# Kernel optimization log

Hardware: AMD Instinct MI355X
Metric: run time of the kernel (lower is better)

The kernel has to match this reference:

```python
import jax, jax.numpy as jnp
from jax import lax
import numpy as np

DN = ('NHWC', 'HWIO', 'NHWC')
BN_EPS = 1e-3  # keras BatchNormalization default epsilon
# 91 threshold candidates, identical to np.arange(0, 0.91, 0.01) in otsu()
THRESH = jnp.asarray(np.arange(0.0, 0.91, 0.01), dtype=jnp.float32)


def _conv(x, w, b, s):
    return lax.conv_general_dilated(x, w, (s, s), 'SAME', dimension_numbers=DN) + b


def _convT(x, w, b, s):
    return lax.conv_transpose(x, w, (s, s), 'SAME', dimension_numbers=DN) + b


def _bn(x, p):
    g, be, m, v = p  # gamma, beta, moving_mean, moving_var (inference mode)
    return (x - m) * lax.rsqrt(v + BN_EPS) * g + be


def _otsu(error):
    # Vectorized equivalent of the nested-python-loop otsu(): for each batch
    # element, find eps in THRESH maximizing p0*p1*(mean0-mean1)^2 where
    # class0 = {err < eps}. Implemented as histogram + cumsums + argmax.
    B, n, m = error.shape
    N = n * m
    K = THRESH.shape[0]
    nb = K + 1  # bin K holds err >= THRESH[-1]
    e = error.reshape(B, N)
    # bins[b,i] = #{k : THRESH[k] <= e[b,i]}  =>  (e < THRESH[k]) <=> (bins <= k)
    bins = jnp.searchsorted(THRESH, e, side='right')
    seg = (jnp.arange(B)[:, None] * nb + bins).reshape(-1)
    counts = jax.ops.segment_sum(jnp.ones(B * N, jnp.float32), seg,
                                 num_segments=B * nb).reshape(B, nb)
    sums = jax.ops.segment_sum(e.reshape(-1), seg,
                               num_segments=B * nb).reshape(B, nb)
    c0 = jnp.cumsum(counts, axis=1)[:, :K]   # |class0| per threshold
    s0 = jnp.cumsum(sums, axis=1)[:, :K]     # sum(class0) per threshold
    tot = jnp.sum(sums, axis=1, keepdims=True)
    p0 = c0 / N
    p1 = 1.0 - p0
    mean0 = s0 / jnp.maximum(c0, 1.0)
    mean1 = (tot - s0) / jnp.maximum(N - c0, 1.0)
    sigma_w = jnp.where((c0 > 0) & (c0 < N), p0 * p1 * (mean0 - mean1) ** 2, 0.0)
    # strict-improvement loop == first argmax; all-zero sigma => threshold 0.0
    return THRESH[jnp.argmax(sigma_w, axis=1)]


def reference(x, eps_z,
              e_w1, e_b1, e_bn1, e_w2, e_b2, e_bn2, e_w3, e_b3, e_bn3,
              e_wm, e_bm, e_wv, e_bv,
              d_wd, d_bd, d_w1, d_b1, d_bn1, d_w2, d_b2, d_bn2,
              d_w3, d_b3, d_bn3, d_w4, d_b4):
    # ---- encoder (Dropout is identity at inference) ----
    h = _bn(jax.nn.relu(_conv(x, e_w1, e_b1, 2)), e_bn1)   # [B,16,16,32]
    h = _bn(jax.nn.relu(_conv(h, e_w2, e_b2, 2)), e_bn2)   # [B,8,8,64]
    h = _bn(jax.nn.relu(_conv(h, e_w3, e_b3, 2)), e_bn3)   # [B,4,4,128]
    h = h.reshape(h.shape[0], -1)                           # [B,2048]
    z_mean = jax.nn.relu(h @ e_wm + e_bm)
    z_log_var = jax.nn.relu(h @ e_wv + e_bv)
    z = z_mean + jnp.exp(0.5 * z_log_var) * eps_z           # Sampling layer
    # ---- decoder ----
    d = jax.nn.relu(z @ d_wd + d_bd).reshape(-1, 8, 8, 128)
    d = _bn(jax.nn.relu(_convT(d, d_w1, d_b1, 1)), d_bn1)   # [B,8,8,128]
    d = _bn(jax.nn.relu(_convT(d, d_w2, d_b2, 2)), d_bn2)   # [B,16,16,64]
    d = _bn(jax.nn.relu(_convT(d, d_w3, d_b3, 2)), d_bn3)   # [B,32,32,32]
    recon = jax.nn.sigmoid(_convT(d, d_w4, d_b4, 1))        # [B,32,32,3]
    # ---- per-pixel error + Otsu threshold + discriminative labelling ----
    error = jnp.mean((x - recon) ** 2, axis=-1)             # [B,32,32]
    thr = _otsu(error)                                      # [B]
    mask = (error < thr[:, None, None]).astype(jnp.int32)   # [B,32,32]
    return mask


def setup_inputs() -> dict:
    key = jax.random.key(0)
    ks = jax.random.split(key, 12)
    B = 2048
    p = lambda k, s: 0.05 * jax.random.normal(k, s, jnp.float32)
    bn = lambda c: (jnp.ones(c, jnp.float32), jnp.zeros(c, jnp.float32),
                    jnp.zeros(c, jnp.float32), jnp.ones(c, jnp.float32))
    return dict(
        x=jax.random.uniform(ks[0], (B, 32, 32, 3), jnp.float32),
        eps_z=jax.random.normal(ks[1], (B, 128), jnp.float32),
        e_w1=p(ks[2], (5, 5, 3, 32)), e_b1=jnp.zeros(32, jnp.float32), e_bn1=bn(32),
        e_w2=p(ks[3], (5, 5, 32, 64)), e_b2=jnp.zeros(64, jnp.float32), e_bn2=bn(64),
        e_w3=p(ks[4], (5, 5, 64, 128)), e_b3=jnp.zeros(128, jnp.float32), e_bn3=bn(128),
        e_wm=p(ks[5], (2048, 128)), e_bm=jnp.zeros(128, jnp.float32),
        e_wv=p(ks[6], (2048, 128)), e_bv=jnp.zeros(128, jnp.float32),
        d_wd=p(ks[7], (128, 8192)), d_bd=jnp.zeros(8192, jnp.float32),
        d_w1=p(ks[8], (1, 1, 128, 128)), d_b1=jnp.zeros(128, jnp.float32), d_bn1=bn(128),
        d_w2=p(ks[9], (3, 3, 128, 64)), d_b2=jnp.zeros(64, jnp.float32), d_bn2=bn(64),
        d_w3=p(ks[10], (3, 3, 64, 32)), d_b3=jnp.zeros(32, jnp.float32), d_bn3=bn(32),
        d_w4=p(ks[11], (3, 3, 32, 3)), d_b4=jnp.zeros(3, jnp.float32),
    )
```

## Files before the change

### kernel.cpp

```cpp
#include <hip/hip_runtime.h>
#include <math.h>

#define B_TOTAL 2048


__device__ __forceinline__ float bn_fold_scale(float g, float v) {
    return g * (float)(1.0 / sqrt((double)v + 1e-3));
}

__global__ __launch_bounds__(256) void k_conv1(
    const float* __restrict__ x, const float* __restrict__ w,
    const float* __restrict__ bias,
    const float* __restrict__ g, const float* __restrict__ be,
    const float* __restrict__ mm, const float* __restrict__ vv,
    float* __restrict__ out, int b0)
{
    __shared__ __align__(16) float sIn[3072];
    __shared__ __align__(16) float sW[2400];
    __shared__ __align__(16) float sB[32], sS[32], sBi[32];
    int t = threadIdx.x;
    const float* xin = x + (size_t)(b0 + blockIdx.x) * 3072;
    for (int i = t; i < 3072; i += 256) sIn[i] = xin[i];
    for (int i = t; i < 2400; i += 256) sW[i] = w[i];
    if (t < 32) {
        float sc = bn_fold_scale(g[t], vv[t]);
        sS[t] = sc; sBi[t] = be[t] - mm[t] * sc; sB[t] = bias[t];
    }
    __syncthreads();
    int oy = t >> 4, ox = t & 15;
    float patch[75];
#pragma unroll
    for (int kh = 0; kh < 5; ++kh) {
        int iy = 2 * oy - 1 + kh;
#pragma unroll
        for (int kw = 0; kw < 5; ++kw) {
            int ix = 2 * ox - 1 + kw;
            bool v = ((unsigned)iy < 32u) && ((unsigned)ix < 32u);
            int base = (iy * 32 + ix) * 3;
#pragma unroll
            for (int c = 0; c < 3; ++c)
                patch[(kh * 5 + kw) * 3 + c] = v ? sIn[base + c] : 0.0f;
        }
    }
    float acc[32];
#pragma unroll
    for (int i = 0; i < 32; ++i) acc[i] = 0.0f;
#pragma unroll 5
    for (int i = 0; i < 75; ++i) {
        float v = patch[i];
        const float* wr = &sW[i * 32];
#pragma unroll
        for (int q = 0; q < 8; ++q) {
            float wl[4];
            *(float4*)wl = *(const float4*)&wr[q * 4];
            acc[q*4+0] = fmaf(v, wl[0], acc[q*4+0]);
            acc[q*4+1] = fmaf(v, wl[1], acc[q*4+1]);
            acc[q*4+2] = fmaf(v, wl[2], acc[q*4+2]);
            acc[q*4+3] = fmaf(v, wl[3], acc[q*4+3]);
        }
    }
    float* o = out + ((size_t)blockIdx.x * 256 + t) * 32;
#pragma unroll
    for (int q = 0; q < 8; ++q) {
        float ov[4];
#pragma unroll
        for (int j = 0; j < 4; ++j) {
            int c = q * 4 + j;
            float r = fmaxf(acc[c] + sB[c], 0.0f);
            ov[j] = fmaf(r, sS[c], sBi[c]);
        }
        *(float4*)&o[q * 4] = *(float4*)ov;
    }
}

__global__ __launch_bounds__(256) void k_c2g(
    const float* __restrict__ in, const float* __restrict__ w,
    const float* __restrict__ bias,
    const float* __restrict__ g, const float* __restrict__ be,
    const float* __restrict__ mm, const float* __restrict__ vv,
    float* __restrict__ out)
{
    __shared__ __align__(16) float sA[32 * 132];
    __shared__ __align__(16) float sW[32 * 64];
    __shared__ __align__(16) float sB[64], sS[64], sBi[64];
    int t = threadIdx.x;
    int img0 = blockIdx.x * 2;
    if (t < 64) {
        float sc = bn_fold_scale(g[t], vv[t]);
        sS[t] = sc; sBi[t] = be[t] - mm[t] * sc; sB[t] = bias[t];
    }
    const float* in0 = in + (size_t)img0 * 8192;
    int tx = t & 15, ty = t >> 4;
    float acc[8][4];
#pragma unroll
    for (int i = 0; i < 8; ++i)
#pragma unroll
        for (int j = 0; j < 4; ++j) acc[i][j] = 0.0f;

    for (int tap = 0; tap < 25; ++tap) {
        int kh = tap / 5, kw = tap - kh * 5;
        __syncthreads();
        for (int i = t; i < 4096; i += 256) {
            int ci = i & 31, m = i >> 5;
            int im = m >> 6, pix = m & 63;
            int oy = pix >> 3, ox = pix & 7;
            int iy = 2 * oy - 1 + kh, ix = 2 * ox - 1 + kw;
            float v = ((unsigned)iy < 16u && (unsigned)ix < 16u)
                          ? in0[((size_t)im * 256 + iy * 16 + ix) * 32 + ci] : 0.0f;
            sA[ci * 132 + m] = v;
        }
        for (int i = t; i < 2048; i += 256) {
            int co = i & 63, ci = i >> 6;
            sW[ci * 64 + co] = w[((size_t)tap * 32 + ci) * 64 + co];
        }
        __syncthreads();
#pragma unroll 4
        for (int ci = 0; ci < 32; ++ci) {
            float b[4];
            *(float4*)b = *(const float4*)&sW[ci * 64 + tx * 4];
            float a0[4], a1[4];
            *(float4*)a0 = *(const float4*)&sA[ci * 132 + ty * 8];
            *(float4*)a1 = *(const float4*)&sA[ci * 132 + ty * 8 + 4];
#pragma unroll
            for (int mi = 0; mi < 4; ++mi)
#pragma unroll
                for (int j = 0; j < 4; ++j) {
                    acc[mi][j]     = fmaf(a0[mi], b[j], acc[mi][j]);
                    acc[4 + mi][j] = fmaf(a1[mi], b[j], acc[4 + mi][j]);
                }
        }
    }
    int c0 = tx * 4;
    float sc[4], bi[4], bv[4];
#pragma unroll
    for (int j = 0; j < 4; ++j) { sc[j] = sS[c0 + j]; bi[j] = sBi[c0 + j]; bv[j] = sB[c0 + j]; }
#pragma unroll
    for (int mi = 0; mi < 8; ++mi) {
        int m = ty * 8 + mi;
        int im = m >> 6, pix = m & 63;
        float ov[4];
#pragma unroll
        for (int j = 0; j < 4; ++j) {
            float r = fmaxf(acc[mi][j] + bv[j], 0.0f);
            ov[j] = fmaf(r, sc[j], bi[j]);
        }
        *(float4*)&out[((size_t)(img0 + im) * 64 + pix) * 64 + c0] = *(float4*)ov;
    }
}

__global__ __launch_bounds__(256) void k_c3g(
    const float* __restrict__ in, const float* __restrict__ w,
    const float* __restrict__ bias,
    const float* __restrict__ g, const float* __restrict__ be,
    const float* __restrict__ mm, const float* __restrict__ vv,
    float* __restrict__ out)
{
    __shared__ __align__(16) float sA[64 * 68];
    __shared__ __align__(16) float sW[64 * 128];
    __shared__ __align__(16) float sB[128], sS[128], sBi[128];
    int t = threadIdx.x;
    int img0 = blockIdx.x * 4;
    if (t < 128) {
        float sc = bn_fold_scale(g[t], vv[t]);
        sS[t] = sc; sBi[t] = be[t] - mm[t] * sc; sB[t] = bias[t];
    }
    const float* in0 = in + (size_t)img0 * 4096;
    int tx = t & 15, ty = t >> 4;
    float acc[4][8];
#pragma unroll
    for (int i = 0; i < 4; ++i)
#pragma unroll
        for (int j = 0; j < 8; ++j) acc[i][j] = 0.0f;

    for (int tap = 0; tap < 25; ++tap) {
        int kh = tap / 5, kw = tap - kh * 5;
        __syncthreads();
        for (int i = t; i < 4096; i += 256) {
            int ci = i & 63, m = i >> 6;
            int im = m >> 4, pix = m & 15;
            int oy = pix >> 2, ox = pix & 3;
            int iy = 2 * oy - 1 + kh, ix = 2 * ox - 1 + kw;
            float v = ((unsigned)iy < 8u && (unsigned)ix < 8u)
                          ? in0[((size_t)im * 64 + iy * 8 + ix) * 64 + ci] : 0.0f;
            sA[ci * 68 + m] = v;
        }
        for (int i = t; i < 8192; i += 256) {
            int co = i & 127, ci = i >> 7;
            sW[ci * 128 + co] = w[((size_t)tap * 64 + ci) * 128 + co];
        }
        __syncthreads();
#pragma unroll 2
        for (int ci = 0; ci < 64; ++ci) {
            float b[8];
            *(float4*)&b[0] = *(const float4*)&sW[ci * 128 + tx * 4];
            *(float4*)&b[4] = *(const float4*)&sW[ci * 128 + 64 + tx * 4];
            float a[4];
            *(float4*)a = *(const float4*)&sA[ci * 68 + ty * 4];
#pragma unroll
            for (int mi = 0; mi < 4; ++mi)
#pragma unroll
                for (int j = 0; j < 8; ++j)
                    acc[mi][j] = fmaf(a[mi], b[j], acc[mi][j]);
        }
    }
    int cA = tx * 4, cB = 64 + tx * 4;
#pragma unroll
    for (int mi = 0; mi < 4; ++mi) {
        int m = ty * 4 + mi;
        int im = m >> 4, pix = m & 15;
        float* o = &out[((size_t)(img0 + im) * 16 + pix) * 128];
        float ov0[4], ov1[4];
#pragma unroll
        for (int j = 0; j < 4; ++j) {
            float r = fmaxf(acc[mi][j] + sB[cA + j], 0.0f);
            ov0[j] = fmaf(r, sS[cA + j], sBi[cA + j]);
        }
#pragma unroll
        for (int j = 0; j < 4; ++j) {
            float r = fmaxf(acc[mi][4 + j] + sB[cB + j], 0.0f);
            ov1[j] = fmaf(r, sS[cB + j], sBi[cB + j]);
        }
        *(float4*)&o[cA] = *(float4*)ov0;
        *(float4*)&o[cB] = *(float4*)ov1;
    }
}

__global__ __launch_bounds__(256) void k_zpart(
    const float* __restrict__ A, const float* __restrict__ Wm,
    const float* __restrict__ Wv, float* __restrict__ part)
{
    __shared__ __align__(16) float sA[16 * 33];
    __shared__ __align__(16) float sW[32 * 256];
    int t = threadIdx.x;
    int img0 = blockIdx.x * 16;
    int k00 = blockIdx.y * 256;
    int li = t >> 4, cg = t & 15;
    float acc[16];
#pragma unroll
    for (int i = 0; i < 16; ++i) acc[i] = 0.0f;
    for (int k0 = 0; k0 < 256; k0 += 32) {
        for (int i = t; i < 512; i += 256) {
            int r = i >> 5, k = i & 31;
            sA[r * 33 + k] = A[(size_t)(img0 + r) * 2048 + k00 + k0 + k];
        }
        for (int i = t; i < 8192; i += 256) {
            int k = i >> 8, c = i & 255;
            float v = (c < 128) ? Wm[(size_t)(k00 + k0 + k) * 128 + c]
                                : Wv[(size_t)(k00 + k0 + k) * 128 + (c - 128)];
            sW[k * 256 + c] = v;
        }
        __syncthreads();
#pragma unroll 4
        for (int k = 0; k < 32; ++k) {
            float a = sA[li * 33 + k];
            const float* wr = &sW[k * 256];
#pragma unroll
            for (int q = 0; q < 4; ++q) {
                float wl[4];
                *(float4*)wl = *(const float4*)&wr[q * 64 + cg * 4];
                acc[q*4+0] = fmaf(a, wl[0], acc[q*4+0]);
                acc[q*4+1] = fmaf(a, wl[1], acc[q*4+1]);
                acc[q*4+2] = fmaf(a, wl[2], acc[q*4+2]);
                acc[q*4+3] = fmaf(a, wl[3], acc[q*4+3]);
            }
        }
        __syncthreads();
    }
    float* p = part + ((size_t)(img0 + li) * 8 + blockIdx.y) * 256;
#pragma unroll
    for (int q = 0; q < 4; ++q) {
        float4 v = make_float4(acc[q*4], acc[q*4+1], acc[q*4+2], acc[q*4+3]);
        *(float4*)&p[q * 64 + cg * 4] = v;
    }
}

__global__ __launch_bounds__(256) void k_zcombine(
    const float* __restrict__ part, const float* __restrict__ bm,
    const float* __restrict__ bv, const float* __restrict__ eps,
    float* __restrict__ z, int b0)
{
    int idx = blockIdx.x * 256 + threadIdx.x;
    int img = idx >> 7, c = idx & 127;
    const float* p = part + (size_t)img * 2048;
    float sm = 0.f, sv = 0.f;
#pragma unroll
    for (int s = 0; s < 8; ++s) { sm += p[s * 256 + c]; sv += p[s * 256 + 128 + c]; }
    float zm = fmaxf(sm + bm[c], 0.0f);
    float zlv = fmaxf(sv + bv[c], 0.0f);
    z[idx] = zm + expf(0.5f * zlv) * eps[(size_t)(b0 + img) * 128 + c];
}

__global__ __launch_bounds__(256) void k_gemm128(
    const float* __restrict__ A, const float* __restrict__ W,
    const float* __restrict__ bias,
    const float* __restrict__ g, const float* __restrict__ be,
    const float* __restrict__ mm, const float* __restrict__ vv,
    float* __restrict__ out, int N, int M)
{
    __shared__ __align__(16) float sAt[64 * 68];
    __shared__ __align__(16) float sB[64 * 68];
    int t = threadIdx.x;
    int tx = t & 15, ty = t >> 4;
    int row0 = blockIdx.x * 64, col0 = blockIdx.y * 64;
    float acc[16];
#pragma unroll
    for (int i = 0; i < 16; ++i) acc[i] = 0.0f;
    for (int kc = 0; kc < 128; kc += 64) {
        for (int i = t; i < 4096; i += 256) {
            int r = i >> 6, k = i & 63;
            sAt[k * 68 + r] = (row0 + r < M) ? A[(size_t)(row0 + r) * 128 + kc + k] : 0.0f;
        }
        for (int i = t; i < 4096; i += 256) {
            int k = i >> 6, c = i & 63;
            sB[k * 68 + c] = W[(size_t)(kc + k) * N + col0 + c];
        }
        __syncthreads();
#pragma unroll 8
        for (int k = 0; k < 64; ++k) {
            float a[4], b[4];
            *(float4*)a = *(const float4*)&sAt[k * 68 + ty * 4];
            *(float4*)b = *(const float4*)&sB[k * 68 + tx * 4];
#pragma unroll
            for (int i = 0; i < 4; ++i)
#pragma unroll
                for (int j = 0; j < 4; ++j)
                    acc[i * 4 + j] = fmaf(a[i], b[j], acc[i * 4 + j]);
        }
        __syncthreads();
    }
    int c0 = col0 + tx * 4;
    float bvv[4];
    *(float4*)bvv = *(const float4*)&bias[c0];
    float sc[4], bi[4];
    bool has_bn = (g != nullptr);
    if (has_bn) {
#pragma unroll
        for (int j = 0; j < 4; ++j) {
            float s = bn_fold_scale(g[c0 + j], vv[c0 + j]);
            sc[j] = s; bi[j] = be[c0 + j] - mm[c0 + j] * s;
        }
    }
#pragma unroll
    for (int i = 0; i < 4; ++i) {
        int row = row0 + ty * 4 + i;
        if (row >= M) continue;
        float ov[4];
#pragma unroll
        for (int j = 0; j < 4; ++j) {
            float r = fmaxf(acc[i * 4 + j] + bvv[j], 0.0f);
            ov[j] = has_bn ? fmaf(r, sc[j], bi[j]) : r;
        }
        *(float4*)&out[(size_t)row * N + c0] = *(float4*)ov;
    }
}

template <int RY, int RX>
__device__ __forceinline__ void ct2g_body(
    const float* __restrict__ in0, const float* __restrict__ w,
    float* __restrict__ sA, float* __restrict__ sW,
    const float* __restrict__ sB, const float* __restrict__ sS,
    const float* __restrict__ sBi, float* __restrict__ out0)
{
    constexpr int NTY = RY ? 1 : 2;
    constexpr int NTX = RX ? 1 : 2;
    constexpr int TT = NTY * NTX;
    int t = threadIdx.x;
    int px0 = (t & 1) * 4;
    int py  = (t >> 1) & 7;
    int u   = (t >> 4) & 1;
    int ty  = t >> 5;
    int co0 = ty * 8;
    int imgA = 2 * u, imgB = 2 * u + 1;
    float acc0[4][8], acc1[4][8];
#pragma unroll
    for (int i = 0; i < 4; ++i)
#pragma unroll
        for (int j = 0; j < 8; ++j) { acc0[i][j] = 0.0f; acc1[i][j] = 0.0f; }

    for (int pass = 0; pass < 8; ++pass) {
        int ci0 = pass * 16;
        __syncthreads();
        for (int img = 0; img < 4; ++img) {
            const float* xin = in0 + (size_t)img * 8192;
            for (int i = t; i < 16 * 81; i += 256) {
                int ci = i & 15, pix = i >> 4;
                int r = pix / 9, c = pix - r * 9;
                int iy = r - 1, ix = c - 1;
                float v = (iy >= 0 && ix >= 0) ? xin[(iy * 8 + ix) * 128 + ci0 + ci] : 0.0f;
                sA[(img * 16 + ci) * 81 + pix] = v;
            }
        }
        for (int tb = 0; tb < TT; tb += 2) {
            if (tb) __syncthreads();
            for (int i = t; i < 2 * 16 * 64; i += 256) {
                int kk = i >> 6, co = i & 63;
                int tl = kk >> 4, ci = kk & 15;
                int tt = tb + tl; if (tt >= TT) tt = TT - 1;
                int kh = RY ? 1 : 2 * (tt / NTX);
                int kw = RX ? 1 : 2 * (tt % NTX);
                sW[kk * 64 + co] = w[((size_t)(kh * 3 + kw) * 128 + ci0 + ci) * 64 + co];
            }
            __syncthreads();
#pragma unroll
            for (int tl = 0; tl < 2; ++tl) {
                int tt = tb + tl;
                if (tt >= TT) break;
                int tY = tt / NTX, tX = tt % NTX;
                int r = RY ? (py + 1) : (py + tY);
                int cb = RX ? (px0 + 1) : (px0 + tX);
                int aB = r * 9 + cb;
#pragma unroll 4
                for (int ci = 0; ci < 16; ++ci) {
                    float b[8];
                    *(float4*)&b[0] = *(const float4*)&sW[(tl * 16 + ci) * 64 + co0];
                    *(float4*)&b[4] = *(const float4*)&sW[(tl * 16 + ci) * 64 + co0 + 4];
                    float a0[4], a1[4];
                    const float* pA = &sA[(imgA * 16 + ci) * 81 + aB];
                    const float* pB = &sA[(imgB * 16 + ci) * 81 + aB];
                    a0[0] = pA[0]; a0[1] = pA[1]; a0[2] = pA[2]; a0[3] = pA[3];
                    a1[0] = pB[0]; a1[1] = pB[1]; a1[2] = pB[2]; a1[3] = pB[3];
#pragma unroll
                    for (int i = 0; i < 4; ++i)
#pragma unroll
                        for (int j = 0; j < 8; ++j) {
                            acc0[i][j] = fmaf(a0[i], b[j], acc0[i][j]);
                            acc1[i][j] = fmaf(a1[i], b[j], acc1[i][j]);
                        }
                }
            }
        }
    }
#pragma unroll
    for (int l = 0; l < 2; ++l) {
        int img = 2 * u + l;
        float* oimg = out0 + (size_t)img * 16384;
#pragma unroll
        for (int i = 0; i < 4; ++i) {
            int oy = 2 * py + RY, ox = 2 * (px0 + i) + RX;
            float* o = oimg + (oy * 16 + ox) * 64 + co0;
            float ov0[4], ov1[4];
#pragma unroll
            for (int j = 0; j < 4; ++j) {
                int c = co0 + j;
                float r = fmaxf((l ? acc1[i][j] : acc0[i][j]) + sB[c], 0.0f);
                ov0[j] = fmaf(r, sS[c], sBi[c]);
            }
#pragma unroll
            for (int j = 0; j < 4; ++j) {
                int c = co0 + 4 + j;
                float r = fmaxf((l ? acc1[i][4 + j] : acc0[i][4 + j]) + sB[c], 0.0f);
                ov1[j] = fmaf(r, sS[c], sBi[c]);
            }
            *(float4*)o = *(float4*)ov0;
            *(float4*)(o + 4) = *(float4*)ov1;
        }
    }
}

__global__ __launch_bounds__(256, 4) void k_ct2g(
    const float* __restrict__ in, const float* __restrict__ w,
    const float* __restrict__ bias,
    const float* __restrict__ g, const float* __restrict__ be,
    const float* __restrict__ mm, const float* __restrict__ vv,
    float* __restrict__ out)
{
    __shared__ __align__(16) float sA[4 * 16 * 81];
    __shared__ __align__(16) float sW[2 * 16 * 64];
    __shared__ __align__(16) float sB[64], sS[64], sBi[64];
    int t = threadIdx.x;
    if (t < 64) {
        float sc = bn_fold_scale(g[t], vv[t]);
        sS[t] = sc; sBi[t] = be[t] - mm[t] * sc; sB[t] = bias[t];
    }
    const float* in0 = in + (size_t)blockIdx.x * 4 * 8192;
    float* out0 = out + (size_t)blockIdx.x * 4 * 16384;
    switch (blockIdx.y) {
        case 0:  ct2g_body<0,0>(in0, w, sA, sW, sB, sS, sBi, out0); break;
        case 1:  ct2g_body<0,1>(in0, w, sA, sW, sB, sS, sBi, out0); break;
        case 2:  ct2g_body<1,0>(in0, w, sA, sW, sB, sS, sBi, out0); break;
        default: ct2g_body<1,1>(in0, w, sA, sW, sB, sS, sBi, out0); break;
    }
}

template <int RY, int RX>
__device__ __forceinline__ void ct3g_body(
    const float* __restrict__ in0, const float* __restrict__ w,
    float* __restrict__ sA, float* __restrict__ sW,
    const float* __restrict__ sB, const float* __restrict__ sS,
    const float* __restrict__ sBi, float* __restrict__ out0)
{
    constexpr int NTY = RY ? 1 : 2;
    constexpr int NTX = RX ? 1 : 2;
    constexpr int TT = NTY * NTX;
    int t = threadIdx.x;
    int px0 = (t & 3) * 4;
    int py  = (t >> 2) & 15;
    int ty  = t >> 6;
    int co0 = ty * 8;
    float acc0[4][8], acc1[4][8];
#pragma unroll
    for (int i = 0; i < 4; ++i)
#pragma unroll
        for (int j = 0; j < 8; ++j) { acc0[i][j] = 0.0f; acc1[i][j] = 0.0f; }

    for (int pass = 0; pass < 8; ++pass) {
        int ci0 = pass * 8;
        __syncthreads();
        for (int img = 0; img < 2; ++img) {
            const float* xin = in0 + (size_t)img * 16384;
            for (int i = t; i < 8 * 289; i += 256) {
                int ci = i & 7, pix = i >> 3;
                int r = pix / 17, c = pix - r * 17;
                int iy = r - 1, ix = c - 1;
                float v = (iy >= 0 && ix >= 0) ? xin[(iy * 16 + ix) * 64 + ci0 + ci] : 0.0f;
                sA[(img * 8 + ci) * 289 + pix] = v;
            }
        }
        for (int tb = 0; tb < TT; tb += 2) {
            if (tb) __syncthreads();
            for (int i = t; i < 2 * 8 * 32; i += 256) {
                int kk = i >> 5, co = i & 31;
                int tl = kk >> 3, ci = kk & 7;
                int tt = tb + tl; if (tt >= TT) tt = TT - 1;
                int kh = RY ? 1 : 2 * (tt / NTX);
                int kw = RX ? 1 : 2 * (tt % NTX);
                sW[kk * 32 + co] = w[((size_t)(kh * 3 + kw) * 64 + ci0 + ci) * 32 + co];
            }
            __syncthreads();
#pragma unroll
            for (int tl = 0; tl < 2; ++tl) {
                int tt = tb + tl;
                if (tt >= TT) break;
                int tY = tt / NTX, tX = tt % NTX;
                int r = RY ? (py + 1) : (py + tY);
                int cb = RX ? (px0 + 1) : (px0 + tX);
                int aB = r * 17 + cb;
#pragma unroll 4
                for (int ci = 0; ci < 8; ++ci) {
                    float b[8];
                    *(float4*)&b[0] = *(const float4*)&sW[(tl * 8 + ci) * 32 + co0];
                    *(float4*)&b[4] = *(const float4*)&sW[(tl * 8 + ci) * 32 + co0 + 4];
                    float a0[4], a1[4];
                    const float* pA = &sA[ci * 289 + aB];
                    const float* pB = &sA[(8 + ci) * 289 + aB];
                    a0[0] = pA[0]; a0[1] = pA[1]; a0[2] = pA[2]; a0[3] = pA[3];
                    a1[0] = pB[0]; a1[1] = pB[1]; a1[2] = pB[2]; a1[3] = pB[3];
#pragma unroll
                    for (int i = 0; i < 4; ++i)
#pragma unroll
                        for (int j = 0; j < 8; ++j) {
                            acc0[i][j] = fmaf(a0[i], b[j], acc0[i][j]);
                            acc1[i][j] = fmaf(a1[i], b[j], acc1[i][j]);
                        }
                }
            }
        }
    }
#pragma unroll
    for (int l = 0; l < 2; ++l) {
        float* oimg = out0 + (size_t)l * 32768;
#pragma unroll
        for (int i = 0; i < 4; ++i) {
            int oy = 2 * py + RY, ox = 2 * (px0 + i) + RX;
            float* o = oimg + (oy * 32 + ox) * 32 + co0;
            float ov0[4], ov1[4];
#pragma unroll
            for (int j = 0; j < 4; ++j) {
                int c = co0 + j;
                float r = fmaxf((l ? acc1[i][j] : acc0[i][j]) + sB[c], 0.0f);
                ov0[j] = fmaf(r, sS[c], sBi[c]);
            }
#pragma unroll
            for (int j = 0; j < 4; ++j) {
                int c = co0 + 4 + j;
                float r = fmaxf((l ? acc1[i][4 + j] : acc0[i][4 + j]) + sB[c], 0.0f);
                ov1[j] = fmaf(r, sS[c], sBi[c]);
            }
            *(float4*)o = *(float4*)ov0;
            *(float4*)(o + 4) = *(float4*)ov1;
        }
    }
}

__global__ __launch_bounds__(256, 4) void k_ct3g(
    const float* __restrict__ in, const float* __restrict__ w,
    const float* __restrict__ bias,
    const float* __restrict__ g, const float* __restrict__ be,
    const float* __restrict__ mm, const float* __restrict__ vv,
    float* __restrict__ out)
{
    __shared__ __align__(16) float sA[2 * 8 * 289];
    __shared__ __align__(16) float sW[2 * 8 * 32];
    __shared__ __align__(16) float sB[32], sS[32], sBi[32];
    int t = threadIdx.x;
    if (t < 32) {
        float sc = bn_fold_scale(g[t], vv[t]);
        sS[t] = sc; sBi[t] = be[t] - mm[t] * sc; sB[t] = bias[t];
    }
    const float* in0 = in + (size_t)blockIdx.x * 2 * 16384;
    float* out0 = out + (size_t)blockIdx.x * 2 * 32768;
    switch (blockIdx.y) {
        case 0:  ct3g_body<0,0>(in0, w, sA, sW, sB, sS, sBi, out0); break;
        case 1:  ct3g_body<0,1>(in0, w, sA, sW, sB, sS, sBi, out0); break;
        case 2:  ct3g_body<1,0>(in0, w, sA, sW, sB, sS, sBi, out0); break;
        default: ct3g_body<1,1>(in0, w, sA, sW, sB, sS, sBi, out0); break;
    }
}

__global__ __launch_bounds__(256) void k_convT4_err(
    const float* __restrict__ in, const float* __restrict__ w,
    const float* __restrict__ b, const float* __restrict__ x,
    float* __restrict__ err, int b0)
{
    __shared__ __align__(16) float sIn[32 * 342];
    int t = threadIdx.x;
    int quart = blockIdx.x, img = blockIdx.y;
    int r0 = quart * 8;
    const float* xin = in + (size_t)img * 32768;
    for (int i = t; i < 10880; i += 256) {
        int pix = i >> 5, ci = i & 31;
        int lr = pix / 34;
        int cx = pix - lr * 34 - 1;
        int gy = r0 - 1 + lr;
        float v = (((unsigned)gy < 32u) && ((unsigned)cx < 32u))
                      ? xin[(gy * 32 + cx) * 32 + ci] : 0.0f;
        sIn[ci * 342 + pix] = v;
    }
    __syncthreads();
    int ly = t >> 5, lx = t & 31;
    float a0 = 0.f, a1 = 0.f, a2 = 0.f;
#pragma unroll
    for (int kh = 0; kh < 3; ++kh)
#pragma unroll
        for (int kw = 0; kw < 3; ++kw) {
            int pix = (ly + kh) * 34 + (lx + kw);
            const float* wp = w + ((kh * 3 + kw) * 32) * 3;
#pragma unroll 4
            for (int ci = 0; ci < 32; ++ci) {
                float v = sIn[ci * 342 + pix];
                a0 = fmaf(v, wp[ci * 3 + 0], a0);
                a1 = fmaf(v, wp[ci * 3 + 1], a1);
                a2 = fmaf(v, wp[ci * 3 + 2], a2);
            }
        }
    float s0 = 1.0f / (1.0f + expf(-(a0 + b[0])));
    float s1 = 1.0f / (1.0f + expf(-(a1 + b[1])));
    float s2 = 1.0f / (1.0f + expf(-(a2 + b[2])));
    int oy = r0 + ly;
    size_t xi = (((size_t)(b0 + img) * 32 + oy) * 32 + lx) * 3;
    float d0 = x[xi + 0] - s0;
    float d1 = x[xi + 1] - s1;
    float d2 = x[xi + 2] - s2;
    err[(size_t)img * 1024 + oy * 32 + lx] = (d0 * d0 + d1 * d1 + d2 * d2) * (1.0f / 3.0f);
}

__global__ __launch_bounds__(256) void k_otsu(
    const float* __restrict__ err, int* __restrict__ mask)
{
    __shared__ float sE[1024];
    __shared__ float sRed[4];
    __shared__ float sSig[96];
    __shared__ float sThr;
    int img = blockIdx.x, t = threadIdx.x;
    const float* e = err + (size_t)img * 1024;
    float part = 0.f;
    for (int i = t; i < 1024; i += 256) { float v = e[i]; sE[i] = v; part += v; }
    for (int o = 32; o; o >>= 1) part += __shfl_down(part, o);
    if ((t & 63) == 0) sRed[t >> 6] = part;
    __syncthreads();
    float tot = sRed[0] + sRed[1] + sRed[2] + sRed[3];
    if (t < 91) {
        float T = (float)((double)t * 0.01);
        int c = 0; float s = 0.f;
        for (int i = 0; i < 1024; ++i) {
            float v = sE[i];
            bool lt = v < T;
            c += lt ? 1 : 0;
            s += lt ? v : 0.0f;
        }
        float cf = (float)c;
        float p0 = cf * (1.0f / 1024.0f);
        float p1 = 1.0f - p0;
        float m0 = s / fmaxf(cf, 1.0f);
        float m1 = (tot - s) / fmaxf(1024.0f - cf, 1.0f);
        float d = m0 - m1;
        sSig[t] = (c > 0 && c < 1024) ? (p0 * p1) * (d * d) : 0.0f;
    }
    __syncthreads();
    if (t == 0) {
        float best = sSig[0]; int bk = 0;
        for (int k = 1; k < 91; ++k)
            if (sSig[k] > best) { best = sSig[k]; bk = k; }
        sThr = (float)((double)bk * 0.01);
    }
    __syncthreads();
    float thr = sThr;
    int* m = mask + (size_t)img * 1024;
    for (int i = t; i < 1024; i += 256) m[i] = (sE[i] < thr) ? 1 : 0;
}

extern "C" void kernel_launch(void* const* d_in, const int* in_sizes, int n_in,
                              void* d_out, int out_size, void* d_ws, size_t ws_size,
                              hipStream_t stream)
{
    (void)in_sizes; (void)out_size;
    const float* p[46];
    bool flat = (n_in >= 46);
    if (flat) {
        for (int i = 0; i < 46; ++i) p[i] = (const float*)d_in[i];
    } else {
        int o = 0;
        int s = 0;
        auto leaf = [&](int count) {
            for (int j = 0; j < count; ++j) p[o++] = (const float*)d_in[s++];
        };
        auto bn4 = [&](int C) {
            const float* base = (const float*)d_in[s++];
            p[o++] = base; p[o++] = base + C; p[o++] = base + 2 * C; p[o++] = base + 3 * C;
        };
        leaf(2);
        leaf(2); bn4(32);
        leaf(2); bn4(64);
        leaf(2); bn4(128);
        leaf(4);
        leaf(2);
        leaf(2); bn4(128);
        leaf(2); bn4(64);
        leaf(2); bn4(32);
        leaf(2);
    }
    const float* x      = p[0];
    const float* epsz   = p[1];
    const float* e_w1   = p[2];
    const float* e_b1   = p[3];
    const float* e_bn1g = p[4], *e_bn1b = p[5], *e_bn1m = p[6], *e_bn1v = p[7];
    const float* e_w2   = p[8];
    const float* e_b2   = p[9];
    const float* e_bn2g = p[10], *e_bn2b = p[11], *e_bn2m = p[12], *e_bn2v = p[13];
    const float* e_w3   = p[14];
    const float* e_b3   = p[15];
    const float* e_bn3g = p[16], *e_bn3b = p[17], *e_bn3m = p[18], *e_bn3v = p[19];
    const float* e_wm   = p[20];
    const float* e_bm   = p[21];
    const float* e_wv   = p[22];
    const float* e_bv   = p[23];
    const float* d_wd   = p[24];
    const float* d_bd   = p[25];
    const float* d_w1   = p[26];
    const float* d_b1   = p[27];
    const float* d_bn1g = p[28], *d_bn1b = p[29], *d_bn1m = p[30], *d_bn1v = p[31];
    const float* d_w2   = p[32];
    const float* d_b2   = p[33];
    const float* d_bn2g = p[34], *d_bn2b = p[35], *d_bn2m = p[36], *d_bn2v = p[37];
    const float* d_w3   = p[38];
    const float* d_b3   = p[39];
    const float* d_bn3g = p[40], *d_bn3b = p[41], *d_bn3m = p[42], *d_bn3v = p[43];
    const float* d_w4   = p[44];
    const float* d_b4   = p[45];
    int* mask = (int*)d_out;

    float* ws = (float*)d_ws;
    int Bc = B_TOTAL;
    while (Bc > 16) {
        size_t need = (size_t)Bc * 50304u * 4u;
        if (need <= ws_size) break;
        Bc >>= 1;
    }
    float* err = ws;
    float* z   = err + (size_t)Bc * 1024;
    float* P   = z + (size_t)Bc * 128;
    float* Q   = P + (size_t)Bc * 16384;

    for (int b0 = 0; b0 < B_TOTAL; b0 += Bc) {
        k_conv1<<<Bc, 256, 0, stream>>>(x, e_w1, e_b1, e_bn1g, e_bn1b, e_bn1m, e_bn1v, P, b0);
        k_c2g<<<Bc / 2, 256, 0, stream>>>(P, e_w2, e_b2, e_bn2g, e_bn2b, e_bn2m, e_bn2v, Q);
        k_c3g<<<Bc / 4, 256, 0, stream>>>(Q, e_w3, e_b3, e_bn3g, e_bn3b, e_bn3m, e_bn3v, P);
        k_zpart<<<dim3(Bc / 16, 8), 256, 0, stream>>>(P, e_wm, e_wv, Q);
        k_zcombine<<<(Bc * 128) / 256, 256, 0, stream>>>(Q, e_bm, e_bv, epsz, z, b0);
        k_gemm128<<<dim3((Bc + 63) / 64, 128), 256, 0, stream>>>(z, d_wd, d_bd,
            nullptr, nullptr, nullptr, nullptr, P, 8192, Bc);
        k_gemm128<<<dim3(Bc, 2), 256, 0, stream>>>(P, d_w1, d_b1,
            d_bn1g, d_bn1b, d_bn1m, d_bn1v, Q, 128, Bc * 64);
        k_ct2g<<<dim3(Bc / 4, 4), 256, 0, stream>>>(Q, d_w2, d_b2, d_bn2g, d_bn2b, d_bn2m, d_bn2v, P);
        k_ct3g<<<dim3(Bc / 2, 4), 256, 0, stream>>>(P, d_w3, d_b3, d_bn3g, d_bn3b, d_bn3m, d_bn3v, Q);
        k_convT4_err<<<dim3(4, Bc), 256, 0, stream>>>(Q, d_w4, d_b4, x, err, b0);
        k_otsu<<<Bc, 256, 0, stream>>>(err, mask + (size_t)b0 * 1024);
    }
}
```

Before: 2.246 ms.

## Prefetch next tap's conv3 input and weights into registers during compute

The conv3 kernel now loads the next tap's im2col input slice and weight slice from global memory into registers (48 floats per thread) while the current tap is being computed. The registers are stored to shared memory at the start of the next iteration. This is meant to hide global-load latency behind the FMA loop, at the cost of higher register pressure, which may reduce occupancy or cause spills.

```diff
diff --git a/kernel.cpp b/kernel.cpp
--- a/kernel.cpp
+++ b/kernel.cpp
@@ -172,21 +172,60 @@
 #pragma unroll
         for (int j = 0; j < 8; ++j) acc[i][j] = 0.0f;
 
-    for (int tap = 0; tap < 25; ++tap) {
-        int kh = tap / 5, kw = tap - kh * 5;
-        __syncthreads();
-        for (int i = t; i < 4096; i += 256) {
+    float aReg[16], wReg[32];
+    {
+        int kh = 0, kw = 0;
+#pragma unroll
+        for (int r = 0; r < 16; ++r) {
+            int i = t + r * 256;
             int ci = i & 63, m = i >> 6;
             int im = m >> 4, pix = m & 15;
             int oy = pix >> 2, ox = pix & 3;
             int iy = 2 * oy - 1 + kh, ix = 2 * ox - 1 + kw;
-            float v = ((unsigned)iy < 8u && (unsigned)ix < 8u)
+            aReg[r] = ((unsigned)iy < 8u && (unsigned)ix < 8u)
                           ? in0[((size_t)im * 64 + iy * 8 + ix) * 64 + ci] : 0.0f;
-            sA[ci * 68 + m] = v;
-        }
-        for (int i = t; i < 8192; i += 256) {
+        }
+#pragma unroll
+        for (int r = 0; r < 32; ++r) {
+            int i = t + r * 256;
             int co = i & 127, ci = i >> 7;
-            sW[ci * 128 + co] = w[((size_t)tap * 64 + ci) * 128 + co];
+            wReg[r] = w[(size_t)ci * 128 + co];
+        }
+    }
+
+    for (int tap = 0; tap < 25; ++tap) {
+        __syncthreads();
+#pragma unroll
+        for (int r = 0; r < 16; ++r) {
+            int i = t + r * 256;
+            int ci = i & 63, m = i >> 6;
+            sA[ci * 68 + m] = aReg[r];
+        }
+#pragma unroll
+        for (int r = 0; r < 32; ++r) {
+            int i = t + r * 256;
+            int co = i & 127, ci = i >> 7;
+            sW[ci * 128 + co] = wReg[r];
+        }
+        if (tap + 1 < 25) {
+            int nt = tap + 1;
+            int kh = nt / 5, kw = nt - kh * 5;
+#pragma unroll
+            for (int r = 0; r < 16; ++r) {
+                int i = t + r * 256;
+                int ci = i & 63, m = i >> 6;
+                int im = m >> 4, pix = m & 15;
+                int oy = pix >> 2, ox = pix & 3;
+                int iy = 2 * oy - 1 + kh, ix = 2 * ox - 1 + kw;
+                aReg[r] = ((unsigned)iy < 8u && (unsigned)ix < 8u)
+                              ? in0[((size_t)im * 64 + iy * 8 + ix) * 64 + ci] : 0.0f;
+            }
+#pragma unroll
+            for (int r = 0; r < 32; ++r) {
+                int i = t + r * 256;
+                int co = i & 127, ci = i >> 7;
+                wReg[r] = w[((size_t)nt * 64 + ci) * 128 + co];
+            }
         }
         __syncthreads();
 #pragma unroll 2
```

After: 2.101 ms. 6.5% less time.
